# Kernel optimization log

Measured on AMD Instinct MI355X. Metric: run time of the kernel, lower is better.

The kernel has to match this reference:

```python
import jax, jax.numpy as jnp
import numpy as np
from jax import lax

BETA = 0.3

def setup_inputs() -> dict:
    key = jax.random.key(0)
    ks = jax.random.split(key, 5)
    B, C, H, W = 1, 64, 96, 96
    x = jax.random.normal(ks[0], (B, C, H, W), dtype=jnp.float32)
    # d_conv: Conv2d(C, C, k=3, stride=1, padding=2, dilation=2)
    dW = jax.random.normal(ks[1], (C, C, 3, 3), dtype=jnp.float32) * 0.05
    db = jax.random.normal(ks[2], (C,), dtype=jnp.float32) * 0.05
    # conv: Conv2d(C, C, k=1)
    cW = jax.random.normal(ks[3], (C, C, 1, 1), dtype=jnp.float32) * 0.1
    cb = jax.random.normal(ks[4], (C,), dtype=jnp.float32) * 0.05
    return {"x": x, "dW": dW, "db": db, "cW": cW, "cb": cb}

def _conv(x, w, b, padding, dilation):
    y = lax.conv_general_dilated(
        x, w, window_strides=(1, 1),
        padding=[(padding, padding), (padding, padding)],
        rhs_dilation=(dilation, dilation),
        dimension_numbers=("NCHW", "OIHW", "NCHW"))
    return y + b[None, :, None, None]

def reference(x, dW, db, cW, cb):
    B, C, H, W = x.shape
    HW = H * W
    y = _conv(x, dW, db, padding=2, dilation=2)   # (B,C,H,W), same d_conv used for q and k
    v = _conv(x, cW, cb, padding=0, dilation=1).reshape(B, HW, C)
    # NOTE: torch uses raw .reshape (not transpose) for q — faithful here.
    q = y.reshape(B, HW, C)
    k = y.reshape(B, C, HW)
    qk = jnp.einsum("bnc,bcm->bnm", q, k)         # (B,HW,HW)
    qk = jnp.where(jnp.abs(qk) > BETA, qk, 0.0)   # threshold mask (qk*mask)
    att = jax.nn.softmax(qk, axis=-1)
    att = jnp.einsum("bnm,bmc->bnc", att, v)      # (B,HW,C)
    att = att.swapaxes(1, 2).reshape(B, C, H, W)
    return x + att
```

## Files before the change

### kernel.cpp

```cpp
#include <hip/hip_runtime.h>
#include <hip/hip_bf16.h>

#define CC 64
#define HW 9216
#define IMG 96
#define SPLITS 8
#define SPLEN 1152
#define ITERS 18
#define LOG2E 1.44269504f

typedef _Float16 f16;
typedef __attribute__((ext_vector_type(8))) _Float16 f16x8;
typedef __attribute__((ext_vector_type(4))) _Float16 f16x4;
typedef __attribute__((ext_vector_type(4))) float f32x4;
typedef __attribute__((ext_vector_type(16))) float f32x16;

__global__ __launch_bounds__(256) void prepad_kernel(
    const float* __restrict__ x, f16* __restrict__ xt)
{
    __shared__ float tile[64][65];
    const int p0 = blockIdx.x * 64;
    const int t = threadIdx.x;
    const int pl = t & 63;
    const int p = p0 + pl;
    int r = p / 100, c = p % 100;
    bool interior = (r >= 2) && (r < 98) && (c >= 2) && (c < 98);
    int img = (r - 2) * IMG + (c - 2);
    #pragma unroll
    for (int j = 0; j < 16; ++j) {
        int ci = j * 4 + (t >> 6);
        tile[pl][ci] = interior ? x[ci * HW + img] : 0.f;
    }
    __syncthreads();
    const int row16 = t >> 4, chunk = t & 15;
    #pragma unroll
    for (int j = 0; j < 4; ++j) {
        int row = j * 16 + row16;
        int pr = p0 + row;
        if (pr < 10000) {
            f16x4 hv = {(f16)tile[row][chunk * 4 + 0], (f16)tile[row][chunk * 4 + 1],
                        (f16)tile[row][chunk * 4 + 2], (f16)tile[row][chunk * 4 + 3]};
            *(f16x4*)&xt[pr * 64 + chunk * 4] = hv;
        }
    }
}

__global__ __launch_bounds__(256) void conv_mfma_kernel(
    const f16* __restrict__ xt, const float* __restrict__ dW, const float* __restrict__ db,
    const float* __restrict__ cW, const float* __restrict__ cb,
    f16* __restrict__ yq, f16* __restrict__ kt, f16* __restrict__ vt)
{
    __shared__ f16 Wl[9 * 16 * 64];
    __shared__ f16 cWl[16 * 64];

    const int b = blockIdx.x;
    const int mblk = b >> 2, cog = b & 3;
    const int co0 = cog * 16;
    const int t = threadIdx.x;

    #pragma unroll 4
    for (int j = 0; j < 36; ++j) {
        int d = j * 256 + t;
        float val = dW[co0 * 576 + d];
        int co  = d / 576;
        int r   = d - co * 576;
        int ci  = r / 9;
        int tap = r - ci * 9;
        Wl[tap * 1024 + co * 64 + ci] = (f16)val;
    }
    #pragma unroll
    for (int j = 0; j < 4; ++j) {
        int d = j * 256 + t;
        cWl[d] = (f16)cW[co0 * CC + d];
    }
    __syncthreads();

    const int w = t >> 6, L = t & 63, g = L >> 4, c16 = L & 15;
    const int ms = mblk * 64 + w * 16;
    const int h = ms / IMG, wc = ms % IMG;
    const int pb = (h + 2) * 100 + (wc + 2) + c16;

    f16x8 Bf[9][2], Bv[2];
    #pragma unroll
    for (int tap = 0; tap < 9; ++tap)
        #pragma unroll
        for (int kc = 0; kc < 2; ++kc)
            Bf[tap][kc] = *(const f16x8*)&Wl[(tap * 16 + c16) * 64 + g * 8 + kc * 32];
    #pragma unroll
    for (int kc = 0; kc < 2; ++kc)
        Bv[kc] = *(const f16x8*)&cWl[c16 * 64 + g * 8 + kc * 32];

    f32x4 accY = (f32x4){0.f, 0.f, 0.f, 0.f};
    f32x4 accV = (f32x4){0.f, 0.f, 0.f, 0.f};

    #pragma unroll
    for (int tap = 0; tap < 9; ++tap) {
        int kh = tap / 3, kw = tap % 3;
        int toff = (2 * kh - 2) * 100 + (2 * kw - 2);
        const f16* ap = xt + (pb + toff) * 64;
        f16x8 A0 = *(const f16x8*)(ap + g * 8);
        f16x8 A1 = *(const f16x8*)(ap + g * 8 + 32);
        accY = __builtin_amdgcn_mfma_f32_16x16x32_f16(A0, Bf[tap][0], accY, 0, 0, 0);
        accY = __builtin_amdgcn_mfma_f32_16x16x32_f16(A1, Bf[tap][1], accY, 0, 0, 0);
        if (tap == 4) {
            accV = __builtin_amdgcn_mfma_f32_16x16x32_f16(A0, Bv[0], accV, 0, 0, 0);
            accV = __builtin_amdgcn_mfma_f32_16x16x32_f16(A1, Bv[1], accV, 0, 0, 0);
        }
    }

    const float dbv = db[co0 + c16], cbv = cb[co0 + c16];
    f16 hy[4];
    #pragma unroll
    for (int j = 0; j < 4; ++j) hy[j] = (f16)(accY[j] + dbv);
    *(f16x4*)&yq[(co0 + c16) * HW + ms + 4 * g] = (f16x4){hy[0], hy[1], hy[2], hy[3]};
    #pragma unroll
    for (int j = 0; j < 4; ++j)
        kt[(ms + 4 * g + j) * 64 + co0 + c16] = hy[j];
    #pragma unroll
    for (int j = 0; j < 4; ++j) {
        int m = ms + 4 * g + j;
        vt[(m & 63) * HW + (co0 + c16) * 144 + (m >> 6)] = (f16)(accV[j] + cbv);
    }
}

__global__ __launch_bounds__(256, 3) void attn_kernel(
    const f16* __restrict__ kt, const f16* __restrict__ vt, const f16* __restrict__ yq,
    f16* __restrict__ acc_ws, float* __restrict__ m_ws, float* __restrict__ l_ws)
{
    __shared__ f16 sKT[64 * 72];
    __shared__ f16 sVT[64 * 72];
    __shared__ f16 sPS[4 * 32 * 72];
    __shared__ float sAL[4 * 32];

    const int t = threadIdx.x;
    const int L = t & 63, w = t >> 6;
    const int l5 = L >> 5, l31 = L & 31;
    const int qb = blockIdx.x >> 3, sp = blockIdx.x & 7;
    const int n0 = qb * 128;
    const int mbase = sp * SPLEN;
    f16* psw = (f16*)sPS + w * 32 * 72;
    float* alw = (float*)sAL + w * 32;

    f16x8 qf[4];
    #pragma unroll
    for (int kc = 0; kc < 4; ++kc)
        qf[kc] = *(const f16x8*)(yq + (n0 + w * 32 + l31) * 64 + kc * 16 + l5 * 8);

    float mi = -1e30f, li = 0.f;
    f32x16 acc[2];
    #pragma unroll
    for (int ct = 0; ct < 2; ++ct)
        #pragma unroll
        for (int r = 0; r < 16; ++r) acc[ct][r] = 0.f;

    for (int it = 0; it < ITERS; ++it) {
        const int m0 = mbase + it * 64;
        __syncthreads();
        #pragma unroll
        for (int rep = 0; rep < 2; ++rep) {
            int idx = t + rep * 256;
            int row = idx >> 3, ch = idx & 7;
            *(uint4*)&sKT[row * 72 + ch * 8] = *(const uint4*)&kt[(m0 + row) * 64 + ch * 8];
            *(uint4*)&sVT[row * 72 + ch * 8] = *(const uint4*)&vt[row * HW + m0 + ch * 8];
        }
        __syncthreads();

        f32x16 st[2];
        #pragma unroll
        for (int kt2 = 0; kt2 < 2; ++kt2) {
            f32x16 d;
            #pragma unroll
            for (int r = 0; r < 16; ++r) d[r] = 0.f;
            #pragma unroll
            for (int kc = 0; kc < 4; ++kc) {
                f16x8 af = *(const f16x8*)&sKT[(kt2 * 32 + l31) * 72 + kc * 16 + l5 * 8];
                d = __builtin_amdgcn_mfma_f32_32x32x16_f16(af, qf[kc], d, 0, 0, 0);
            }
            st[kt2] = d;
        }
        #pragma unroll
        for (int kt2 = 0; kt2 < 2; ++kt2)
            #pragma unroll
            for (int r = 0; r < 16; ++r)
                st[kt2][r] = (fabsf(st[kt2][r]) > 0.3f) ? st[kt2][r] : 0.f;

        float q8[8];
        #pragma unroll
        for (int kt2 = 0; kt2 < 2; ++kt2)
            #pragma unroll
            for (int rq = 0; rq < 4; ++rq)
                q8[kt2 * 4 + rq] = fmaxf(fmaxf(st[kt2][rq * 4 + 0], st[kt2][rq * 4 + 1]),
                                         fmaxf(st[kt2][rq * 4 + 2], st[kt2][rq * 4 + 3]));
        float mx = fmaxf(fmaxf(fmaxf(q8[0], q8[1]), fmaxf(q8[2], q8[3])),
                         fmaxf(fmaxf(q8[4], q8[5]), fmaxf(q8[6], q8[7])));
        mx = fmaxf(mx, __shfl_xor(mx, 32, 64));
        float mnew = fmaxf(mi, mx);
        float nL = mnew * LOG2E;
        float alpha = __builtin_amdgcn_exp2f(mi * LOG2E - nL);
        mi = mnew;

        float ls = 0.f;
        #pragma unroll
        for (int kt2 = 0; kt2 < 2; ++kt2)
            #pragma unroll
            for (int rq = 0; rq < 4; ++rq) {
                float p0 = __builtin_amdgcn_exp2f(fmaf(st[kt2][rq * 4 + 0], LOG2E, -nL));
                float p1 = __builtin_amdgcn_exp2f(fmaf(st[kt2][rq * 4 + 1], LOG2E, -nL));
                float p2 = __builtin_amdgcn_exp2f(fmaf(st[kt2][rq * 4 + 2], LOG2E, -nL));
                float p3 = __builtin_amdgcn_exp2f(fmaf(st[kt2][rq * 4 + 3], LOG2E, -nL));
                ls += (p0 + p1) + (p2 + p3);
                unsigned u0 = __builtin_bit_cast(unsigned int, __builtin_amdgcn_cvt_pkrtz(p0, p1));
                unsigned u1 = __builtin_bit_cast(unsigned int, __builtin_amdgcn_cvt_pkrtz(p2, p3));
                uint2 uv; uv.x = u0; uv.y = u1;
                *(uint2*)&psw[l31 * 72 + kt2 * 32 + rq * 8 + l5 * 4] = uv;
            }
        li = li * alpha + ls;

        if (l5 == 0) alw[l31] = alpha;
        f32x4 aj[4];
        #pragma unroll
        for (int rq = 0; rq < 4; ++rq)
            aj[rq] = *(const f32x4*)&alw[rq * 8 + l5 * 4];
        #pragma unroll
        for (int ct = 0; ct < 2; ++ct)
            #pragma unroll
            for (int r = 0; r < 16; ++r)
                acc[ct][r] *= aj[r >> 2][r & 3];

        f16x8 pa[4];
        #pragma unroll
        for (int kc = 0; kc < 4; ++kc)
            pa[kc] = *(const f16x8*)&psw[l31 * 72 + kc * 16 + l5 * 8];
        #pragma unroll
        for (int ct = 0; ct < 2; ++ct)
            #pragma unroll
            for (int kc = 0; kc < 4; ++kc) {
                f16x8 vb = *(const f16x8*)&sVT[(ct * 32 + l31) * 72 + kc * 16 + l5 * 8];
                acc[ct] = __builtin_amdgcn_mfma_f32_32x32x16_f16(pa[kc], vb, acc[ct], 0, 0, 0);
            }
    }

    float li_tot = li + __shfl_xor(li, 32, 64);

    const int base = blockIdx.x;
    #pragma unroll
    for (int ct = 0; ct < 2; ++ct)
        #pragma unroll
        for (int r = 0; r < 16; ++r) {
            int ql = w * 32 + (r & 3) + 8 * (r >> 2) + 4 * l5;
            int c  = ct * 32 + l31;
            acc_ws[base * 8192 + ql * 64 + c] = (f16)acc[ct][r];
        }
    if (l5 == 0) {
        m_ws[base * 128 + w * 32 + l31] = mi;
        l_ws[base * 128 + w * 32 + l31] = li_tot;
    }
}

__global__ __launch_bounds__(256) void merge_kernel(
    const f16* __restrict__ acc_ws, const float* __restrict__ m_ws, const float* __restrict__ l_ws,
    const float* __restrict__ x, float* __restrict__ out)
{
    __shared__ float wsh[SPLITS * 16];
    __shared__ float att[64 * 17];
    const int b = blockIdx.x;
    const int row0 = b * 16;
    const int qb = row0 >> 7;
    const int ql0 = row0 & 127;
    const int t = threadIdx.x;
    if (t < 16) {
        int ql = ql0 + t;
        float ms = -1e30f;
        float mv[SPLITS];
        #pragma unroll
        for (int sp = 0; sp < SPLITS; ++sp) {
            mv[sp] = m_ws[(qb * SPLITS + sp) * 128 + ql];
            ms = fmaxf(ms, mv[sp]);
        }
        float Lsum = 0.f, ev[SPLITS];
        #pragma unroll
        for (int sp = 0; sp < SPLITS; ++sp) {
            ev[sp] = __builtin_amdgcn_exp2f((mv[sp] - ms) * LOG2E);
            Lsum += l_ws[(qb * SPLITS + sp) * 128 + ql] * ev[sp];
        }
        float inv = 1.f / Lsum;
        #pragma unroll
        for (int sp = 0; sp < SPLITS; ++sp)
            wsh[sp * 16 + t] = ev[sp] * inv;
    }
    __syncthreads();
    for (int i = t; i < 1024; i += 256) {
        int rr = i >> 6, c = i & 63;
        float v = 0.f;
        #pragma unroll
        for (int sp = 0; sp < SPLITS; ++sp)
            v += (float)acc_ws[(qb * SPLITS + sp) * 8192 + (ql0 + rr) * 64 + c] * wsh[sp * 16 + rr];
        att[c * 17 + rr] = v;
    }
    __syncthreads();
    for (int i = t; i < 1024; i += 256) {
        int c = i >> 4, r = i & 15;
        int idx = c * HW + row0 + r;
        out[idx] = x[idx] + att[c * 17 + r];
    }
}

extern "C" void kernel_launch(void* const* d_in, const int* in_sizes, int n_in,
                              void* d_out, int out_size, void* d_ws, size_t ws_size,
                              hipStream_t stream)
{
    const float* x  = (const float*)d_in[0];
    const float* dW = (const float*)d_in[1];
    const float* db = (const float*)d_in[2];
    const float* cW = (const float*)d_in[3];
    const float* cb = (const float*)d_in[4];
    float* out = (float*)d_out;

    char* ws = (char*)d_ws;
    f16* kt     = (f16*)(ws);
    f16* yq     = (f16*)(ws + 1179648);
    f16* vt     = (f16*)(ws + 2359296);
    f16* xt     = (f16*)(ws + 3538944);
    f16* acc_ws = (f16*)(ws + 4818944);
    float* m_ws = (float*)(ws + 14256128);
    float* l_ws = (float*)(ws + 14551040);

    prepad_kernel<<<dim3(157), dim3(256), 0, stream>>>(x, xt);
    conv_mfma_kernel<<<dim3(576), dim3(256), 0, stream>>>(xt, dW, db, cW, cb, yq, kt, vt);
    attn_kernel<<<dim3(72 * SPLITS), dim3(256), 0, stream>>>(kt, vt, yq, acc_ws, m_ws, l_ws);
    merge_kernel<<<dim3(576), dim3(256), 0, stream>>>(acc_ws, m_ws, l_ws, x, out);
}
```

Baseline: 138.2 us.

## Split attention key tile across warp pairs with intra-block softmax merge

Each attention block now covers 64 queries instead of 128, and its four warps form a 2x2 grid: two query halves by two key halves of each 64-key tile. Each warp computes a 32x32 score tile and a half-K PV product, and the two key-half partial states are combined through shared memory at the end. This doubles the grid to 1152 blocks and raises the occupancy hint to 4, aiming for more parallelism and fewer registers per warp. In exchange, each query's K/V tiles are loaded by twice as many blocks, there is an extra reduction step with syncs, and the per-split partial accumulators are rounded to f16 before merging.

New measurement: 142.8 us. +3.3%, slower.

```diff
diff --git a/kernel.cpp b/kernel.cpp
--- a/kernel.cpp
+++ b/kernel.cpp
@@ -123,28 +123,29 @@
     }
 }
 
-__global__ __launch_bounds__(256, 3) void attn_kernel(
+__global__ __launch_bounds__(256, 4) void attn_kernel(
     const f16* __restrict__ kt, const f16* __restrict__ vt, const f16* __restrict__ yq,
     f16* __restrict__ acc_ws, float* __restrict__ m_ws, float* __restrict__ l_ws)
 {
     __shared__ f16 sKT[64 * 72];
     __shared__ f16 sVT[64 * 72];
-    __shared__ f16 sPS[4 * 32 * 72];
+    __shared__ f16 sPS[4 * 32 * 40];
     __shared__ float sAL[4 * 32];
 
     const int t = threadIdx.x;
     const int L = t & 63, w = t >> 6;
     const int l5 = L >> 5, l31 = L & 31;
+    const int qh = w & 1, kh = w >> 1;
     const int qb = blockIdx.x >> 3, sp = blockIdx.x & 7;
-    const int n0 = qb * 128;
+    const int n0 = qb * 64;
     const int mbase = sp * SPLEN;
-    f16* psw = (f16*)sPS + w * 32 * 72;
+    f16* psw = (f16*)sPS + w * 32 * 40;
     float* alw = (float*)sAL + w * 32;
 
     f16x8 qf[4];
     #pragma unroll
     for (int kc = 0; kc < 4; ++kc)
-        qf[kc] = *(const f16x8*)(yq + (n0 + w * 32 + l31) * 64 + kc * 16 + l5 * 8);
+        qf[kc] = *(const f16x8*)(yq + (n0 + qh * 32 + l31) * 64 + kc * 16 + l5 * 8);
 
     float mi = -1e30f, li = 0.f;
     f32x16 acc[2];
@@ -165,34 +166,24 @@
         }
         __syncthreads();
 
-        f32x16 st[2];
-        #pragma unroll
-        for (int kt2 = 0; kt2 < 2; ++kt2) {
-            f32x16 d;
-            #pragma unroll
-            for (int r = 0; r < 16; ++r) d[r] = 0.f;
-            #pragma unroll
-            for (int kc = 0; kc < 4; ++kc) {
-                f16x8 af = *(const f16x8*)&sKT[(kt2 * 32 + l31) * 72 + kc * 16 + l5 * 8];
-                d = __builtin_amdgcn_mfma_f32_32x32x16_f16(af, qf[kc], d, 0, 0, 0);
-            }
-            st[kt2] = d;
-        }
-        #pragma unroll
-        for (int kt2 = 0; kt2 < 2; ++kt2)
-            #pragma unroll
-            for (int r = 0; r < 16; ++r)
-                st[kt2][r] = (fabsf(st[kt2][r]) > 0.3f) ? st[kt2][r] : 0.f;
-
-        float q8[8];
-        #pragma unroll
-        for (int kt2 = 0; kt2 < 2; ++kt2)
-            #pragma unroll
-            for (int rq = 0; rq < 4; ++rq)
-                q8[kt2 * 4 + rq] = fmaxf(fmaxf(st[kt2][rq * 4 + 0], st[kt2][rq * 4 + 1]),
-                                         fmaxf(st[kt2][rq * 4 + 2], st[kt2][rq * 4 + 3]));
-        float mx = fmaxf(fmaxf(fmaxf(q8[0], q8[1]), fmaxf(q8[2], q8[3])),
-                         fmaxf(fmaxf(q8[4], q8[5]), fmaxf(q8[6], q8[7])));
+        f32x16 st;
+        #pragma unroll
+        for (int r = 0; r < 16; ++r) st[r] = 0.f;
+        #pragma unroll
+        for (int kc = 0; kc < 4; ++kc) {
+            f16x8 af = *(const f16x8*)&sKT[(kh * 32 + l31) * 72 + kc * 16 + l5 * 8];
+            st = __builtin_amdgcn_mfma_f32_32x32x16_f16(af, qf[kc], st, 0, 0, 0);
+        }
+        #pragma unroll
+        for (int r = 0; r < 16; ++r)
+            st[r] = (fabsf(st[r]) > 0.3f) ? st[r] : 0.f;
+
+        float q4[4];
+        #pragma unroll
+        for (int rq = 0; rq < 4; ++rq)
+            q4[rq] = fmaxf(fmaxf(st[rq * 4 + 0], st[rq * 4 + 1]),
+                           fmaxf(st[rq * 4 + 2], st[rq * 4 + 3]));
+        float mx = fmaxf(fmaxf(q4[0], q4[1]), fmaxf(q4[2], q4[3]));
         mx = fmaxf(mx, __shfl_xor(mx, 32, 64));
         float mnew = fmaxf(mi, mx);
         float nL = mnew * LOG2E;
@@ -201,19 +192,17 @@
 
         float ls = 0.f;
         #pragma unroll
-        for (int kt2 = 0; kt2 < 2; ++kt2)
-            #pragma unroll
-            for (int rq = 0; rq < 4; ++rq) {
-                float p0 = __builtin_amdgcn_exp2f(fmaf(st[kt2][rq * 4 + 0], LOG2E, -nL));
-                float p1 = __builtin_amdgcn_exp2f(fmaf(st[kt2][rq * 4 + 1], LOG2E, -nL));
-                float p2 = __builtin_amdgcn_exp2f(fmaf(st[kt2][rq * 4 + 2], LOG2E, -nL));
-                float p3 = __builtin_amdgcn_exp2f(fmaf(st[kt2][rq * 4 + 3], LOG2E, -nL));
-                ls += (p0 + p1) + (p2 + p3);
-                unsigned u0 = __builtin_bit_cast(unsigned int, __builtin_amdgcn_cvt_pkrtz(p0, p1));
-                unsigned u1 = __builtin_bit_cast(unsigned int, __builtin_amdgcn_cvt_pkrtz(p2, p3));
-                uint2 uv; uv.x = u0; uv.y = u1;
-                *(uint2*)&psw[l31 * 72 + kt2 * 32 + rq * 8 + l5 * 4] = uv;
-            }
+        for (int rq = 0; rq < 4; ++rq) {
+            float p0 = __builtin_amdgcn_exp2f(fmaf(st[rq * 4 + 0], LOG2E, -nL));
+            float p1 = __builtin_amdgcn_exp2f(fmaf(st[rq * 4 + 1], LOG2E, -nL));
+            float p2 = __builtin_amdgcn_exp2f(fmaf(st[rq * 4 + 2], LOG2E, -nL));
+            float p3 = __builtin_amdgcn_exp2f(fmaf(st[rq * 4 + 3], LOG2E, -nL));
+            ls += (p0 + p1) + (p2 + p3);
+            unsigned u0 = __builtin_bit_cast(unsigned int, __builtin_amdgcn_cvt_pkrtz(p0, p1));
+            unsigned u1 = __builtin_bit_cast(unsigned int, __builtin_amdgcn_cvt_pkrtz(p2, p3));
+            uint2 uv; uv.x = u0; uv.y = u1;
+            *(uint2*)&psw[l31 * 40 + rq * 8 + l5 * 4] = uv;
+        }
         li = li * alpha + ls;
 
         if (l5 == 0) alw[l31] = alpha;
@@ -227,33 +216,78 @@
             for (int r = 0; r < 16; ++r)
                 acc[ct][r] *= aj[r >> 2][r & 3];
 
-        f16x8 pa[4];
-        #pragma unroll
-        for (int kc = 0; kc < 4; ++kc)
-            pa[kc] = *(const f16x8*)&psw[l31 * 72 + kc * 16 + l5 * 8];
+        f16x8 pa[2];
+        #pragma unroll
+        for (int kc2 = 0; kc2 < 2; ++kc2)
+            pa[kc2] = *(const f16x8*)&psw[l31 * 40 + kc2 * 16 + l5 * 8];
         #pragma unroll
         for (int ct = 0; ct < 2; ++ct)
             #pragma unroll
-            for (int kc = 0; kc < 4; ++kc) {
-                f16x8 vb = *(const f16x8*)&sVT[(ct * 32 + l31) * 72 + kc * 16 + l5 * 8];
-                acc[ct] = __builtin_amdgcn_mfma_f32_32x32x16_f16(pa[kc], vb, acc[ct], 0, 0, 0);
+            for (int kc2 = 0; kc2 < 2; ++kc2) {
+                f16x8 vb = *(const f16x8*)&sVT[(ct * 32 + l31) * 72 + kh * 32 + kc2 * 16 + l5 * 8];
+                acc[ct] = __builtin_amdgcn_mfma_f32_32x32x16_f16(pa[kc2], vb, acc[ct], 0, 0, 0);
             }
     }
 
     float li_tot = li + __shfl_xor(li, 32, 64);
 
-    const int base = blockIdx.x;
-    #pragma unroll
-    for (int ct = 0; ct < 2; ++ct)
-        #pragma unroll
-        for (int r = 0; r < 16; ++r) {
-            int ql = w * 32 + (r & 3) + 8 * (r >> 2) + 4 * l5;
-            int c  = ct * 32 + l31;
-            acc_ws[base * 8192 + ql * 64 + c] = (f16)acc[ct][r];
-        }
-    if (l5 == 0) {
-        m_ws[base * 128 + w * 32 + l31] = mi;
-        l_ws[base * 128 + w * 32 + l31] = li_tot;
+    __syncthreads();
+    f16* accx  = (f16*)sPS;
+    float* mix = (float*)((char*)sPS + 8704);
+    float* lix = mix + 64;
+    if (kh == 1) {
+        f16* dst = accx + (qh * 64 + L) * 34;
+        #pragma unroll
+        for (int ct = 0; ct < 2; ++ct)
+            #pragma unroll
+            for (int rq = 0; rq < 4; ++rq) {
+                unsigned u0 = __builtin_bit_cast(unsigned int,
+                    __builtin_amdgcn_cvt_pkrtz(acc[ct][rq * 4 + 0], acc[ct][rq * 4 + 1]));
+                unsigned u1 = __builtin_bit_cast(unsigned int,
+                    __builtin_amdgcn_cvt_pkrtz(acc[ct][rq * 4 + 2], acc[ct][rq * 4 + 3]));
+                uint2 uv; uv.x = u0; uv.y = u1;
+                *(uint2*)(dst + ct * 16 + rq * 4) = uv;
+            }
+        if (l5 == 0) {
+            mix[qh * 32 + l31] = mi;
+            lix[qh * 32 + l31] = li_tot;
+        }
+    }
+    __syncthreads();
+    if (kh == 0) {
+        float mi2 = mix[qh * 32 + l31], li2 = lix[qh * 32 + l31];
+        float mnew = fmaxf(mi, mi2);
+        float e1 = __builtin_amdgcn_exp2f((mi  - mnew) * LOG2E);
+        float e2 = __builtin_amdgcn_exp2f((mi2 - mnew) * LOG2E);
+        float lsum = li_tot * e1 + li2 * e2;
+        if (l5 == 0) {
+            alw[l31] = e1;
+            sAL[(w + 2) * 32 + l31] = e2;
+        }
+        f32x4 a1[4], a2[4];
+        #pragma unroll
+        for (int rq = 0; rq < 4; ++rq) {
+            a1[rq] = *(const f32x4*)&alw[rq * 8 + l5 * 4];
+            a2[rq] = *(const f32x4*)&sAL[(w + 2) * 32 + rq * 8 + l5 * 4];
+        }
+        const f16* src = accx + (qh * 64 + L) * 34;
+        const int base = blockIdx.x;
+        #pragma unroll
+        for (int ct = 0; ct < 2; ++ct) {
+            f16 pr[16];
+            *(f16x8*)&pr[0] = *(const f16x8*)(src + ct * 16);
+            *(f16x8*)&pr[8] = *(const f16x8*)(src + ct * 16 + 8);
+            #pragma unroll
+            for (int r = 0; r < 16; ++r) {
+                float cv = acc[ct][r] * a1[r >> 2][r & 3] + (float)pr[r] * a2[r >> 2][r & 3];
+                int ql = qh * 32 + (r & 3) + 8 * (r >> 2) + 4 * l5;
+                acc_ws[base * 4096 + ql * 64 + ct * 32 + l31] = (f16)cv;
+            }
+        }
+        if (l5 == 0) {
+            m_ws[base * 64 + qh * 32 + l31] = mnew;
+            l_ws[base * 64 + qh * 32 + l31] = lsum;
+        }
     }
 }
 
@@ -263,25 +297,23 @@
 {
     __shared__ float wsh[SPLITS * 16];
     __shared__ float att[64 * 17];
-    const int b = blockIdx.x;
-    const int row0 = b * 16;
-    const int qb = row0 >> 7;
-    const int ql0 = row0 & 127;
+    const int qb = blockIdx.x >> 2, sub = blockIdx.x & 3;
+    const int r0 = sub * 16;
     const int t = threadIdx.x;
     if (t < 16) {
-        int ql = ql0 + t;
+        int row = r0 + t;
         float ms = -1e30f;
         float mv[SPLITS];
         #pragma unroll
         for (int sp = 0; sp < SPLITS; ++sp) {
-            mv[sp] = m_ws[(qb * SPLITS + sp) * 128 + ql];
+            mv[sp] = m_ws[(qb * SPLITS + sp) * 64 + row];
             ms = fmaxf(ms, mv[sp]);
         }
         float Lsum = 0.f, ev[SPLITS];
         #pragma unroll
         for (int sp = 0; sp < SPLITS; ++sp) {
             ev[sp] = __builtin_amdgcn_exp2f((mv[sp] - ms) * LOG2E);
-            Lsum += l_ws[(qb * SPLITS + sp) * 128 + ql] * ev[sp];
+            Lsum += l_ws[(qb * SPLITS + sp) * 64 + row] * ev[sp];
         }
         float inv = 1.f / Lsum;
         #pragma unroll
@@ -294,13 +326,14 @@
         float v = 0.f;
         #pragma unroll
         for (int sp = 0; sp < SPLITS; ++sp)
-            v += (float)acc_ws[(qb * SPLITS + sp) * 8192 + (ql0 + rr) * 64 + c] * wsh[sp * 16 + rr];
+            v += (float)acc_ws[(qb * SPLITS + sp) * 4096 + (r0 + rr) * 64 + c] * wsh[sp * 16 + rr];
         att[c * 17 + rr] = v;
     }
     __syncthreads();
+    const int n0 = qb * 64 + r0;
     for (int i = t; i < 1024; i += 256) {
         int c = i >> 4, r = i & 15;
-        int idx = c * HW + row0 + r;
+        int idx = c * HW + n0 + r;
         out[idx] = x[idx] + att[c * 17 + r];
     }
 }
@@ -327,6 +360,6 @@
 
     prepad_kernel<<<dim3(157), dim3(256), 0, stream>>>(x, xt);
     conv_mfma_kernel<<<dim3(576), dim3(256), 0, stream>>>(xt, dW, db, cW, cb, yq, kt, vt);
-    attn_kernel<<<dim3(72 * SPLITS), dim3(256), 0, stream>>>(kt, vt, yq, acc_ws, m_ws, l_ws);
+    attn_kernel<<<dim3(144 * SPLITS), dim3(256), 0, stream>>>(kt, vt, yq, acc_ws, m_ws, l_ws);
     merge_kernel<<<dim3(576), dim3(256), 0, stream>>>(acc_ws, m_ws, l_ws, x, out);
 }
```
